# Performance work log

Measured on AMD Instinct MI355X. Metric: run time of the kernel, lower is better.

## Reference

```python
import jax, jax.numpy as jnp
import numpy as np

N_HEADS = 8
TANH_CLIPPING = 10.0
TEMP = 1.0


def setup_inputs() -> dict:
    key = jax.random.key(0)
    ks = jax.random.split(key, 8)
    B, N, D, CTX = 256, 1000, 128, 130
    embeddings = jax.random.normal(ks[0], (B, N, D), dtype=jnp.float32)
    step_context = jax.random.normal(ks[1], (B, 1, CTX), dtype=jnp.float32)
    mask = jax.random.randint(ks[2], (B, 1, N), 0, 2).astype(bool)
    # ensure at least one feasible node per row (node 0 always feasible)
    mask = mask.at[:, :, 0].set(False)
    W_node = jax.random.normal(ks[3], (D, 3 * D), dtype=jnp.float32) * (1.0 / np.sqrt(D))
    W_fixed = jax.random.normal(ks[4], (D, D), dtype=jnp.float32) * (1.0 / np.sqrt(D))
    W_step = jax.random.normal(ks[5], (CTX, D), dtype=jnp.float32) * (1.0 / np.sqrt(CTX))
    W_out = jax.random.normal(ks[6], (D, D), dtype=jnp.float32) * (1.0 / np.sqrt(D))
    return {"embeddings": embeddings, "step_context": step_context, "mask": mask,
            "W_node": W_node, "W_fixed": W_fixed, "W_step": W_step, "W_out": W_out}


def reference(embeddings, step_context, mask, W_node, W_fixed, W_step, W_out):
    # embeddings: [B, N, D], step_context: [B, 1, D+2], mask: [B, 1, N] (True = infeasible)
    B, N, D = embeddings.shape
    H = N_HEADS
    hd = D // H
    # _precompute: fixed context from graph mean, and K/V/logit_key from node embeddings
    graph_embed = embeddings.mean(axis=1)                       # [B, D]
    fixed_context = graph_embed @ W_fixed                       # [B, D]
    kvl = embeddings @ W_node                                   # [B, N, 3D]
    glimpse_k, glimpse_v, logit_k = jnp.split(kvl, 3, axis=-1)  # each [B, N, D]
    # query = fixed context + projected step context             [B, 1, D]
    query = fixed_context[:, None, :] + step_context @ W_step
    # multi-head glimpse attention (q_len = 1)
    q = query.reshape(B, 1, H, hd).transpose(0, 2, 1, 3)        # [B, H, 1, hd]
    K = glimpse_k.reshape(B, N, H, hd).transpose(0, 2, 1, 3)    # [B, H, N, hd]
    V = glimpse_v.reshape(B, N, H, hd).transpose(0, 2, 1, 3)    # [B, H, N, hd]
    compat = jnp.einsum('bhqd,bhnd->bhqn', q, K) / jnp.sqrt(jnp.float32(hd))
    # mask_inner
    compat = jnp.where(mask[:, None, :, :], -jnp.inf, compat)
    attn = jax.nn.softmax(compat, axis=-1)                      # [B, H, 1, N]
    heads = jnp.einsum('bhqn,bhnd->bhqd', attn, V)              # [B, H, 1, hd]
    glimpse = heads.transpose(0, 2, 1, 3).reshape(B, 1, D) @ W_out  # [B, 1, D]
    # single-head logits against logit_key, tanh-clipped
    logits = jnp.einsum('bqd,bnd->bqn', glimpse, logit_k) / jnp.sqrt(jnp.float32(D))
    logits = jnp.tanh(logits) * TANH_CLIPPING
    # mask_logits
    logits = jnp.where(mask, -jnp.inf, logits)
    log_p = jax.nn.log_softmax(logits / TEMP, axis=-1)          # [B, 1, N]
    return log_p
```

## Files before the change

kernel.cpp:

```cpp
#include <hip/hip_runtime.h>
#include <math.h>

#define NN   1000
#define DD   128
#define CTXN 130
#define NEG_BIG (-1.0e30f)

__device__ __forceinline__ float fast_tanh(float a) {
    a = fminf(fmaxf(a, -20.f), 20.f);
    const float ex = __expf(-2.0f * a);
    return (1.0f - ex) / (1.0f + ex);
}


__global__ __launch_bounds__(1024, 4)
void k1_fused(const float* __restrict__ emb, const float* __restrict__ stepc,
              const void* __restrict__ maskp,
              const float* __restrict__ Wn, const float* __restrict__ Wf,
              const float* __restrict__ Ws,
              float* __restrict__ qpt, int* __restrict__ idxv, int* __restrict__ cntv) {
    const int b = blockIdx.x, t = threadIdx.x;
    const int w = t >> 6, lane = t & 63;
    const float* eb = emb + (size_t)b * (NN * DD);
    __shared__ __align__(16) float S[4096];
    __shared__ float s_mean[128], s_q[128];
    __shared__ int s_misint;
    __shared__ unsigned long long s_bal[16];
    __shared__ int s_woff[16];
    if (t == 0) {
        const unsigned char* mb8 = (const unsigned char*)maskp;
        int any = 0;
        for (int k = 0; k < 64; ++k) any |= mb8[4 * k + 1];
        s_misint = (any == 0) ? 1 : 0;
    }
    {
        const int c4 = t & 31, g = t >> 5;
        float4 a = make_float4(0.f, 0.f, 0.f, 0.f);
        for (int r = g; r < NN; r += 32) {
            const float4 v = *(const float4*)(eb + (size_t)r * DD + c4 * 4);
            a.x += v.x; a.y += v.y; a.z += v.z; a.w += v.w;
        }
        ((float4*)S)[g * 32 + c4] = a;
    }
    __syncthreads();
    if (t < 128) {
        float v = 0.f;
        #pragma unroll
        for (int g = 0; g < 32; ++g) v += S[g * 128 + t];
        s_mean[t] = v * (1.0f / (float)NN);
    }
    __syncthreads();
    {
        const int d = t & 127, p = t >> 7;
        float a = 0.f;
        for (int i = 16 * p; i < 16 * p + 16; ++i)
            a = fmaf(s_mean[i], Wf[i * DD + d], a);
        const float* scb = stepc + (size_t)b * CTXN;
        const int c0 = 16 * p, c1 = (p == 7) ? CTXN : 16 * p + 16;
        for (int c = c0; c < c1; ++c)
            a = fmaf(scb[c], Ws[c * DD + d], a);
        S[p * 128 + d] = a;
    }
    __syncthreads();
    if (t < 128) {
        float v = 0.f;
        #pragma unroll
        for (int p = 0; p < 8; ++p) v += S[p * 128 + t];
        s_q[t] = v;
    }
    __syncthreads();
    {
        const int i = t & 127, h = t >> 7;
        float a = 0.f;
        #pragma unroll
        for (int j = 0; j < 16; ++j)
            a = fmaf(Wn[i * 384 + h * 16 + j], s_q[h * 16 + j], a);
        qpt[(size_t)b * 1024 + h * 128 + i] = a * 0.25f;
    }
    {
        const unsigned char* mk8 = (const unsigned char*)maskp + (size_t)b * NN;
        const int* mk32 = (const int*)maskp + (size_t)b * NN;
        int um = 0;
        if (t < NN) um = s_misint ? (mk32[t] == 0) : (mk8[t] == 0);
        const unsigned long long bal = __ballot(um);
        if (lane == 0) s_bal[w] = bal;
        __syncthreads();
        if (t == 0) {
            int o = 0;
            #pragma unroll
            for (int w2 = 0; w2 < 16; ++w2) {
                s_woff[w2] = o;
                o += (int)__popcll(s_bal[w2]);
            }
            cntv[b] = o;
        }
        __syncthreads();
        if (um) {
            const int pos = s_woff[w] +
                (int)__popcll(bal & ((lane == 0) ? 0ULL : (~0ULL >> (64 - lane))));
            idxv[(size_t)b * 1024 + pos] = t;
        }
    }
}

__global__ __launch_bounds__(512, 4)
void kB_stream(const float* __restrict__ emb, const float* __restrict__ qpt,
               const float* __restrict__ Wn,
               const int* __restrict__ idxv, const int* __restrict__ cntv,
               float* __restrict__ headsp, float* __restrict__ stats) {
    const int b = blockIdx.x >> 3, s = blockIdx.x & 7;
    const int t = threadIdx.x, w = t >> 6, lane = t & 63;
    const int rg = lane >> 4, cl = lane & 15;
    const int cnt = cntv[b];
    const int lo = (s * cnt) >> 3;
    const int hi = ((s + 1) * cnt) >> 3;
    const int nrows = hi - lo;
    const float* eb = emb + (size_t)b * (NN * DD);
    __shared__ __align__(16) float s_qpT[1024];
    __shared__ __align__(16) float s_part[8 * 8 * 132];
    __shared__ float s_sumw[64];
    __shared__ int s_idx[128];
    for (int i = t; i < 1024; i += 512) s_qpT[i] = qpt[(size_t)b * 1024 + i];
    if (t < 128) s_idx[t] = (t < nrows) ? idxv[(size_t)b * 1024 + lo + t] : 0;
    __syncthreads();
    const int h0 = 2 * rg, h1 = 2 * rg + 1;
    const float4 qa0 = *(const float4*)&s_qpT[h0 * 128 + cl * 8];
    const float4 qa1 = *(const float4*)&s_qpT[h0 * 128 + cl * 8 + 4];
    const float4 qb0 = *(const float4*)&s_qpT[h1 * 128 + cl * 8];
    const float4 qb1 = *(const float4*)&s_qpT[h1 * 128 + cl * 8 + 4];
    float4 a0A = make_float4(0.f,0.f,0.f,0.f), a0B = a0A;
    float4 a1A = a0A, a1B = a0A;
    float ps0 = 0.f, ps1 = 0.f;
    const int mainIt = nrows >> 3;
    for (int it = 0; it < mainIt; ++it) {
        const int rp = it * 8 + w;
        const int n = s_idx[rp];
        const float4 e0 = *(const float4*)(eb + (size_t)n * DD + cl * 8);
        const float4 e1 = *(const float4*)(eb + (size_t)n * DD + cl * 8 + 4);
        float c0 = e0.x * qa0.x;
        c0 = fmaf(e0.y, qa0.y, c0); c0 = fmaf(e0.z, qa0.z, c0); c0 = fmaf(e0.w, qa0.w, c0);
        c0 = fmaf(e1.x, qa1.x, c0); c0 = fmaf(e1.y, qa1.y, c0);
        c0 = fmaf(e1.z, qa1.z, c0); c0 = fmaf(e1.w, qa1.w, c0);
        float c1 = e0.x * qb0.x;
        c1 = fmaf(e0.y, qb0.y, c1); c1 = fmaf(e0.z, qb0.z, c1); c1 = fmaf(e0.w, qb0.w, c1);
        c1 = fmaf(e1.x, qb1.x, c1); c1 = fmaf(e1.y, qb1.y, c1);
        c1 = fmaf(e1.z, qb1.z, c1); c1 = fmaf(e1.w, qb1.w, c1);
        c0 += __shfl_xor(c0, 1, 16); c1 += __shfl_xor(c1, 1, 16);
        c0 += __shfl_xor(c0, 2, 16); c1 += __shfl_xor(c1, 2, 16);
        c0 += __shfl_xor(c0, 4, 16); c1 += __shfl_xor(c1, 4, 16);
        c0 += __shfl_xor(c0, 8, 16); c1 += __shfl_xor(c1, 8, 16);
        const float p0 = __expf(fminf(c0, 80.f));
        const float p1 = __expf(fminf(c1, 80.f));
        ps0 += p0; ps1 += p1;
        a0A.x = fmaf(p0, e0.x, a0A.x); a0A.y = fmaf(p0, e0.y, a0A.y);
        a0A.z = fmaf(p0, e0.z, a0A.z); a0A.w = fmaf(p0, e0.w, a0A.w);
        a0B.x = fmaf(p0, e1.x, a0B.x); a0B.y = fmaf(p0, e1.y, a0B.y);
        a0B.z = fmaf(p0, e1.z, a0B.z); a0B.w = fmaf(p0, e1.w, a0B.w);
        a1A.x = fmaf(p1, e0.x, a1A.x); a1A.y = fmaf(p1, e0.y, a1A.y);
        a1A.z = fmaf(p1, e0.z, a1A.z); a1A.w = fmaf(p1, e0.w, a1A.w);
        a1B.x = fmaf(p1, e1.x, a1B.x); a1B.y = fmaf(p1, e1.y, a1B.y);
        a1B.z = fmaf(p1, e1.z, a1B.z); a1B.w = fmaf(p1, e1.w, a1B.w);
    }
    if (mainIt * 8 < nrows) {
        const int rp = mainIt * 8 + w;
        const bool valid = (rp < nrows);
        const int n = s_idx[rp & 127];
        float4 e0 = make_float4(0.f,0.f,0.f,0.f), e1 = e0;
        if (valid) {
            e0 = *(const float4*)(eb + (size_t)n * DD + cl * 8);
            e1 = *(const float4*)(eb + (size_t)n * DD + cl * 8 + 4);
        }
        float c0 = e0.x * qa0.x;
        c0 = fmaf(e0.y, qa0.y, c0); c0 = fmaf(e0.z, qa0.z, c0); c0 = fmaf(e0.w, qa0.w, c0);
        c0 = fmaf(e1.x, qa1.x, c0); c0 = fmaf(e1.y, qa1.y, c0);
        c0 = fmaf(e1.z, qa1.z, c0); c0 = fmaf(e1.w, qa1.w, c0);
        float c1 = e0.x * qb0.x;
        c1 = fmaf(e0.y, qb0.y, c1); c1 = fmaf(e0.z, qb0.z, c1); c1 = fmaf(e0.w, qb0.w, c1);
        c1 = fmaf(e1.x, qb1.x, c1); c1 = fmaf(e1.y, qb1.y, c1);
        c1 = fmaf(e1.z, qb1.z, c1); c1 = fmaf(e1.w, qb1.w, c1);
        c0 += __shfl_xor(c0, 1, 16); c1 += __shfl_xor(c1, 1, 16);
        c0 += __shfl_xor(c0, 2, 16); c1 += __shfl_xor(c1, 2, 16);
        c0 += __shfl_xor(c0, 4, 16); c1 += __shfl_xor(c1, 4, 16);
        c0 += __shfl_xor(c0, 8, 16); c1 += __shfl_xor(c1, 8, 16);
        const float p0 = valid ? __expf(fminf(c0, 80.f)) : 0.f;
        const float p1 = valid ? __expf(fminf(c1, 80.f)) : 0.f;
        ps0 += p0; ps1 += p1;
        a0A.x = fmaf(p0, e0.x, a0A.x); a0A.y = fmaf(p0, e0.y, a0A.y);
        a0A.z = fmaf(p0, e0.z, a0A.z); a0A.w = fmaf(p0, e0.w, a0A.w);
        a0B.x = fmaf(p0, e1.x, a0B.x); a0B.y = fmaf(p0, e1.y, a0B.y);
        a0B.z = fmaf(p0, e1.z, a0B.z); a0B.w = fmaf(p0, e1.w, a0B.w);
        a1A.x = fmaf(p1, e0.x, a1A.x); a1A.y = fmaf(p1, e0.y, a1A.y);
        a1A.z = fmaf(p1, e0.z, a1A.z); a1A.w = fmaf(p1, e0.w, a1A.w);
        a1B.x = fmaf(p1, e1.x, a1B.x); a1B.y = fmaf(p1, e1.y, a1B.y);
        a1B.z = fmaf(p1, e1.z, a1B.z); a1B.w = fmaf(p1, e1.w, a1B.w);
    }
    *(float4*)&s_part[(w * 8 + h0) * 132 + cl * 8]     = a0A;
    *(float4*)&s_part[(w * 8 + h0) * 132 + cl * 8 + 4] = a0B;
    *(float4*)&s_part[(w * 8 + h1) * 132 + cl * 8]     = a1A;
    *(float4*)&s_part[(w * 8 + h1) * 132 + cl * 8 + 4] = a1B;
    if (cl == 0) { s_sumw[w * 8 + h0] = ps0; s_sumw[w * 8 + h1] = ps1; }
    __syncthreads();
    float vres0, vres1;
    {
        const int i0 = t, i1 = t + 512;
        const int hA = i0 >> 7, cA = i0 & 127;
        const int hB = i1 >> 7, cB = i1 & 127;
        float v0 = 0.f, v1 = 0.f;
        #pragma unroll
        for (int w2 = 0; w2 < 8; ++w2) {
            v0 += s_part[(w2 * 8 + hA) * 132 + cA];
            v1 += s_part[(w2 * 8 + hB) * 132 + cB];
        }
        vres0 = v0; vres1 = v1;
    }
    __syncthreads();
    s_part[t]       = vres0;
    s_part[t + 512] = vres1;
    __syncthreads();
    {
        const int j = t & 127, p = t >> 7;
        const int h = j >> 4;
        float a = 0.f;
        for (int i = 32 * p; i < 32 * p + 32; ++i)
            a = fmaf(Wn[i * 384 + 128 + j], s_part[h * 128 + i], a);
        s_part[1024 + p * 128 + j] = a;
    }
    __syncthreads();
    if (t < 128)
        headsp[(size_t)b * 1024 + s * 128 + t] =
            s_part[1024 + t] + s_part[1024 + 128 + t] +
            s_part[1024 + 256 + t] + s_part[1024 + 384 + t];
    if (t < 8) {
        float v = 0.f;
        #pragma unroll
        for (int w2 = 0; w2 < 8; ++w2) v += s_sumw[w2 * 8 + t];
        stats[(size_t)b * 64 + s * 8 + t] = v;
    }
}

__global__ __launch_bounds__(1024, 4)
void k4_fused(const float* __restrict__ emb, const float* __restrict__ headsp,
              const float* __restrict__ stats,
              const float* __restrict__ Wn, const float* __restrict__ Wo,
              const int* __restrict__ idxv, const int* __restrict__ cntv,
              float* __restrict__ out) {
    const int b = blockIdx.x, t = threadIdx.x;
    const int w = t >> 6, lane = t & 63;
    const int rg = lane >> 4, cl = lane & 15;
    const float* eb = emb + (size_t)b * (NN * DD);
    __shared__ float s_dinv[8];
    __shared__ __align__(16) float s_red[1024];
    __shared__ float s_h[128], s_gl[128], s_g2[128];
    __shared__ float s_logits[1000];
    __shared__ int s_idxf[1024];
    __shared__ float s_r2[32];
    __shared__ float s_lse;
    const int cnt = cntv[b];
    if (t < NN) s_logits[t] = NEG_BIG;
    s_idxf[t] = (t < cnt) ? idxv[(size_t)b * 1024 + t] : 0;
    if (t < 8) {
        float den = 0.f;
        #pragma unroll
        for (int ss = 0; ss < 8; ++ss) den += stats[(size_t)b * 64 + ss * 8 + t];
        s_dinv[t] = 1.0f / den;
    }
    __syncthreads();
    if (t < 128) {
        float v = 0.f;
        #pragma unroll
        for (int ss = 0; ss < 8; ++ss) v += headsp[(size_t)b * 1024 + ss * 128 + t];
        s_h[t] = v * s_dinv[t >> 4];
    }
    __syncthreads();
    {
        const int d = t & 127, p = t >> 7;
        float a = 0.f;
        for (int j = 16 * p; j < 16 * p + 16; ++j)
            a = fmaf(s_h[j], Wo[j * DD + d], a);
        s_red[p * 128 + d] = a;
    }
    __syncthreads();
    if (t < 128) {
        float v = 0.f;
        #pragma unroll
        for (int p = 0; p < 8; ++p) v += s_red[p * 128 + t];
        s_gl[t] = v;
    }
    __syncthreads();
    {
        const int i = t & 127, p = t >> 7;
        float a = 0.f;
        for (int d = 16 * p; d < 16 * p + 16; ++d)
            a = fmaf(Wn[i * 384 + 256 + d], s_gl[d], a);
        s_red[p * 128 + i] = a;
    }
    __syncthreads();
    if (t < 128) {
        float v = 0.f;
        #pragma unroll
        for (int p = 0; p < 8; ++p) v += s_red[p * 128 + t];
        s_g2[t] = v * 0.08838834764831845f;
    }
    __syncthreads();
    {
        const float4 ga = *(const float4*)&s_g2[cl * 8];
        const float4 gb = *(const float4*)&s_g2[cl * 8 + 4];
        const int mainL = cnt >> 6;
        for (int it = 0; it < mainL; ++it) {
            const int pos = it * 64 + w * 4 + rg;
            const int n = s_idxf[pos];
            const float4 e0 = *(const float4*)(eb + (size_t)n * DD + cl * 8);
            const float4 e1 = *(const float4*)(eb + (size_t)n * DD + cl * 8 + 4);
            float a = e0.x * ga.x;
            a = fmaf(e0.y, ga.y, a);
            a = fmaf(e0.z, ga.z, a);
            a = fmaf(e0.w, ga.w, a);
            a = fmaf(e1.x, gb.x, a);
            a = fmaf(e1.y, gb.y, a);
            a = fmaf(e1.z, gb.z, a);
            a = fmaf(e1.w, gb.w, a);
            a += __shfl_xor(a, 1, 16);
            a += __shfl_xor(a, 2, 16);
            a += __shfl_xor(a, 4, 16);
            a += __shfl_xor(a, 8, 16);
            if (cl == 0)
                s_logits[n] = 10.0f * fast_tanh(a);
        }
        if (mainL * 64 < cnt) {
            const int pos = mainL * 64 + w * 4 + rg;
            const bool valid = (pos < cnt);
            const int n = s_idxf[pos & 1023];
            float a = 0.f;
            if (valid) {
                const float4 e0 = *(const float4*)(eb + (size_t)n * DD + cl * 8);
                const float4 e1 = *(const float4*)(eb + (size_t)n * DD + cl * 8 + 4);
                a = e0.x * ga.x;
                a = fmaf(e0.y, ga.y, a);
                a = fmaf(e0.z, ga.z, a);
                a = fmaf(e0.w, ga.w, a);
                a = fmaf(e1.x, gb.x, a);
                a = fmaf(e1.y, gb.y, a);
                a = fmaf(e1.z, gb.z, a);
                a = fmaf(e1.w, gb.w, a);
            }
            a += __shfl_xor(a, 1, 16);
            a += __shfl_xor(a, 2, 16);
            a += __shfl_xor(a, 4, 16);
            a += __shfl_xor(a, 8, 16);
            if (cl == 0 && valid)
                s_logits[n] = 10.0f * fast_tanh(a);
        }
    }
    __syncthreads();
    {
        float sum = (t < NN) ? __expf(s_logits[t]) : 0.f;
        #pragma unroll
        for (int o = 32; o; o >>= 1) sum += __shfl_xor(sum, o, 64);
        if (lane == 0) s_r2[w] = sum;
        __syncthreads();
        if (t == 0) {
            float ss = 0.f;
            #pragma unroll
            for (int i = 0; i < 16; ++i) ss += s_r2[i];
            s_lse = logf(ss);
        }
        __syncthreads();
        if (t < NN) out[(size_t)b * NN + t] = s_logits[t] - s_lse;
    }
}

extern "C" void kernel_launch(void* const* d_in, const int* in_sizes, int n_in,
                              void* d_out, int out_size, void* d_ws, size_t ws_size,
                              hipStream_t stream) {
    const float* emb   = (const float*)d_in[0];
    const float* stepc = (const float*)d_in[1];
    const void*  mask  = (const void*)d_in[2];
    const float* Wn = (const float*)d_in[3];
    const float* Wf = (const float*)d_in[4];
    const float* Ws = (const float*)d_in[5];
    const float* Wo = (const float*)d_in[6];
    float* out = (float*)d_out;
    const int B = in_sizes[0] / (NN * DD);

    float* wsf = (float*)d_ws;
    const size_t n_qpt   = (size_t)B * 1024;
    const size_t n_hp    = (size_t)B * 1024;
    const size_t n_stats = (size_t)B * 64;
    const size_t n_idx   = (size_t)B * 1024;

    float* qpt    = wsf;
    float* headsp = qpt + n_qpt;
    float* stats  = headsp + n_hp;
    int*   idxv   = (int*)(stats + n_stats);
    int*   cntv   = idxv + n_idx;

    k1_fused <<<B,     1024, 0, stream>>>(emb, stepc, mask, Wn, Wf, Ws, qpt, idxv, cntv);
    kB_stream<<<B * 8, 512,  0, stream>>>(emb, qpt, Wn, idxv, cntv, headsp, stats);
    k4_fused <<<B,     1024, 0, stream>>>(emb, headsp, stats, Wn, Wo, idxv, cntv, out);
}
```

Before: 78.31 us.

## Split graph-mean pass across 8 blocks per batch and recompute query/index lists per block

The first kernel, which ran one 1024-thread block per batch row to read all embeddings for the mean, becomes a lightweight partial-sum kernel launched with 8 blocks per batch row. This raises parallelism for the full-embedding read. The query projection and the compaction of feasible node indices move into the streaming kernel, and each of its 8 blocks per batch row recomputes them redundantly. The final kernel rebuilds the index list from the mask itself. The qpt/idxv/cnt global round trips go away in exchange for redundant per-block matrix-vector work and mask scans.

```diff
diff --git a/kernel.cpp b/kernel.cpp
--- a/kernel.cpp
+++ b/kernel.cpp
@@ -13,116 +13,124 @@
 }
 
 
-__global__ __launch_bounds__(1024, 4)
-void k1_fused(const float* __restrict__ emb, const float* __restrict__ stepc,
-              const void* __restrict__ maskp,
-              const float* __restrict__ Wn, const float* __restrict__ Wf,
-              const float* __restrict__ Ws,
-              float* __restrict__ qpt, int* __restrict__ idxv, int* __restrict__ cntv) {
-    const int b = blockIdx.x, t = threadIdx.x;
-    const int w = t >> 6, lane = t & 63;
+__global__ __launch_bounds__(256, 8)
+void k1p_meanpart(const float* __restrict__ emb, float* __restrict__ meanp) {
+    const int b = blockIdx.x >> 3, s = blockIdx.x & 7;
+    const int t = threadIdx.x;
     const float* eb = emb + (size_t)b * (NN * DD);
-    __shared__ __align__(16) float S[4096];
-    __shared__ float s_mean[128], s_q[128];
-    __shared__ int s_misint;
+    __shared__ __align__(16) float s_red[8 * 128];
+    const int c4 = t & 31, rg = t >> 5;
+    float4 a = make_float4(0.f, 0.f, 0.f, 0.f);
+    for (int nl = rg; nl < 125; nl += 8) {
+        const float4 v = *(const float4*)(eb + (size_t)(s * 125 + nl) * DD + c4 * 4);
+        a.x += v.x; a.y += v.y; a.z += v.z; a.w += v.w;
+    }
+    ((float4*)s_red)[rg * 32 + c4] = a;
+    __syncthreads();
+    if (t < 128) {
+        float v = 0.f;
+        #pragma unroll
+        for (int g = 0; g < 8; ++g) v += s_red[g * 128 + t];
+        meanp[(size_t)b * 1024 + s * 128 + t] = v;
+    }
+}
+
+__global__ __launch_bounds__(512, 4)
+void kB_stream(const float* __restrict__ emb, const float* __restrict__ meanp,
+               const float* __restrict__ stepc, const void* __restrict__ maskp,
+               const float* __restrict__ Wn, const float* __restrict__ Wf,
+               const float* __restrict__ Ws,
+               float* __restrict__ headsp, float* __restrict__ stats) {
+    const int b = blockIdx.x >> 3, s = blockIdx.x & 7;
+    const int t = threadIdx.x, w = t >> 6, lane = t & 63;
+    const int rg = lane >> 4, cl = lane & 15;
+    const float* eb = emb + (size_t)b * (NN * DD);
+    __shared__ __align__(16) float s_qpT[1024];
+    __shared__ __align__(16) float s_part[8 * 8 * 132];
+    __shared__ float s_sumw[64];
+    __shared__ int s_idx[128];
     __shared__ unsigned long long s_bal[16];
     __shared__ int s_woff[16];
+    __shared__ int s_cnt, s_misint;
+    float* s_mean = s_part;
+    float* s_q    = s_part + 128;
+    float* s_scr  = s_part + 256;
     if (t == 0) {
         const unsigned char* mb8 = (const unsigned char*)maskp;
         int any = 0;
         for (int k = 0; k < 64; ++k) any |= mb8[4 * k + 1];
         s_misint = (any == 0) ? 1 : 0;
     }
-    {
-        const int c4 = t & 31, g = t >> 5;
-        float4 a = make_float4(0.f, 0.f, 0.f, 0.f);
-        for (int r = g; r < NN; r += 32) {
-            const float4 v = *(const float4*)(eb + (size_t)r * DD + c4 * 4);
-            a.x += v.x; a.y += v.y; a.z += v.z; a.w += v.w;
-        }
-        ((float4*)S)[g * 32 + c4] = a;
-    }
-    __syncthreads();
     if (t < 128) {
         float v = 0.f;
         #pragma unroll
-        for (int g = 0; g < 32; ++g) v += S[g * 128 + t];
+        for (int g = 0; g < 8; ++g) v += meanp[(size_t)b * 1024 + g * 128 + t];
         s_mean[t] = v * (1.0f / (float)NN);
     }
     __syncthreads();
     {
         const int d = t & 127, p = t >> 7;
         float a = 0.f;
-        for (int i = 16 * p; i < 16 * p + 16; ++i)
+        for (int i = 32 * p; i < 32 * p + 32; ++i)
             a = fmaf(s_mean[i], Wf[i * DD + d], a);
         const float* scb = stepc + (size_t)b * CTXN;
-        const int c0 = 16 * p, c1 = (p == 7) ? CTXN : 16 * p + 16;
+        const int c0 = 32 * p, c1 = (p == 3) ? CTXN : 32 * p + 32;
         for (int c = c0; c < c1; ++c)
             a = fmaf(scb[c], Ws[c * DD + d], a);
-        S[p * 128 + d] = a;
-    }
-    __syncthreads();
-    if (t < 128) {
-        float v = 0.f;
-        #pragma unroll
-        for (int p = 0; p < 8; ++p) v += S[p * 128 + t];
-        s_q[t] = v;
-    }
-    __syncthreads();
-    {
-        const int i = t & 127, h = t >> 7;
-        float a = 0.f;
-        #pragma unroll
-        for (int j = 0; j < 16; ++j)
-            a = fmaf(Wn[i * 384 + h * 16 + j], s_q[h * 16 + j], a);
-        qpt[(size_t)b * 1024 + h * 128 + i] = a * 0.25f;
+        s_scr[p * 128 + d] = a;
+    }
+    __syncthreads();
+    if (t < 128) s_q[t] = s_scr[t] + s_scr[128 + t] + s_scr[256 + t] + s_scr[384 + t];
+    __syncthreads();
+    {
+        const int i = t & 127, p = t >> 7;
+        #pragma unroll
+        for (int u = 0; u < 2; ++u) {
+            const int h = p + 4 * u;
+            float a = 0.f;
+            #pragma unroll
+            for (int j = 0; j < 16; ++j)
+                a = fmaf(Wn[i * 384 + h * 16 + j], s_q[h * 16 + j], a);
+            s_qpT[h * 128 + i] = a * 0.25f;
+        }
     }
     {
         const unsigned char* mk8 = (const unsigned char*)maskp + (size_t)b * NN;
         const int* mk32 = (const int*)maskp + (size_t)b * NN;
-        int um = 0;
-        if (t < NN) um = s_misint ? (mk32[t] == 0) : (mk8[t] == 0);
-        const unsigned long long bal = __ballot(um);
-        if (lane == 0) s_bal[w] = bal;
+        const int misint = s_misint;
+        #pragma unroll
+        for (int r = 0; r < 2; ++r) {
+            const int gi = r * 512 + t;
+            int um = 0;
+            if (gi < NN) um = misint ? (mk32[gi] == 0) : (mk8[gi] == 0);
+            const unsigned long long bal = __ballot(um);
+            if (lane == 0) s_bal[r * 8 + w] = bal;
+        }
         __syncthreads();
         if (t == 0) {
             int o = 0;
             #pragma unroll
-            for (int w2 = 0; w2 < 16; ++w2) {
-                s_woff[w2] = o;
-                o += (int)__popcll(s_bal[w2]);
+            for (int k = 0; k < 16; ++k) { s_woff[k] = o; o += (int)__popcll(s_bal[k]); }
+            s_cnt = o;
+        }
+        __syncthreads();
+        const int cnt = s_cnt;
+        const int lo = (s * cnt) >> 3, hi = ((s + 1) * cnt) >> 3;
+        #pragma unroll
+        for (int r = 0; r < 2; ++r) {
+            const int gi = r * 512 + t;
+            const unsigned long long bal = s_bal[r * 8 + w];
+            if ((bal >> lane) & 1ULL) {
+                const int pos = s_woff[r * 8 + w] +
+                    (int)__popcll(bal & ((lane == 0) ? 0ULL : (~0ULL >> (64 - lane))));
+                if (pos >= lo && pos < hi) s_idx[pos - lo] = gi;
             }
-            cntv[b] = o;
-        }
-        __syncthreads();
-        if (um) {
-            const int pos = s_woff[w] +
-                (int)__popcll(bal & ((lane == 0) ? 0ULL : (~0ULL >> (64 - lane))));
-            idxv[(size_t)b * 1024 + pos] = t;
-        }
-    }
-}
-
-__global__ __launch_bounds__(512, 4)
-void kB_stream(const float* __restrict__ emb, const float* __restrict__ qpt,
-               const float* __restrict__ Wn,
-               const int* __restrict__ idxv, const int* __restrict__ cntv,
-               float* __restrict__ headsp, float* __restrict__ stats) {
-    const int b = blockIdx.x >> 3, s = blockIdx.x & 7;
-    const int t = threadIdx.x, w = t >> 6, lane = t & 63;
-    const int rg = lane >> 4, cl = lane & 15;
-    const int cnt = cntv[b];
-    const int lo = (s * cnt) >> 3;
-    const int hi = ((s + 1) * cnt) >> 3;
+        }
+    }
+    __syncthreads();
+    const int cnt = s_cnt;
+    const int lo = (s * cnt) >> 3, hi = ((s + 1) * cnt) >> 3;
     const int nrows = hi - lo;
-    const float* eb = emb + (size_t)b * (NN * DD);
-    __shared__ __align__(16) float s_qpT[1024];
-    __shared__ __align__(16) float s_part[8 * 8 * 132];
-    __shared__ float s_sumw[64];
-    __shared__ int s_idx[128];
-    for (int i = t; i < 1024; i += 512) s_qpT[i] = qpt[(size_t)b * 1024 + i];
-    if (t < 128) s_idx[t] = (t < nrows) ? idxv[(size_t)b * 1024 + lo + t] : 0;
-    __syncthreads();
     const int h0 = 2 * rg, h1 = 2 * rg + 1;
     const float4 qa0 = *(const float4*)&s_qpT[h0 * 128 + cl * 8];
     const float4 qa1 = *(const float4*)&s_qpT[h0 * 128 + cl * 8 + 4];
@@ -194,6 +202,7 @@
         a1B.x = fmaf(p1, e1.x, a1B.x); a1B.y = fmaf(p1, e1.y, a1B.y);
         a1B.z = fmaf(p1, e1.z, a1B.z); a1B.w = fmaf(p1, e1.w, a1B.w);
     }
+    __syncthreads();
     *(float4*)&s_part[(w * 8 + h0) * 132 + cl * 8]     = a0A;
     *(float4*)&s_part[(w * 8 + h0) * 132 + cl * 8 + 4] = a0B;
     *(float4*)&s_part[(w * 8 + h1) * 132 + cl * 8]     = a1A;
@@ -240,9 +249,8 @@
 
 __global__ __launch_bounds__(1024, 4)
 void k4_fused(const float* __restrict__ emb, const float* __restrict__ headsp,
-              const float* __restrict__ stats,
+              const float* __restrict__ stats, const void* __restrict__ maskp,
               const float* __restrict__ Wn, const float* __restrict__ Wo,
-              const int* __restrict__ idxv, const int* __restrict__ cntv,
               float* __restrict__ out) {
     const int b = blockIdx.x, t = threadIdx.x;
     const int w = t >> 6, lane = t & 63;
@@ -255,9 +263,16 @@
     __shared__ int s_idxf[1024];
     __shared__ float s_r2[32];
     __shared__ float s_lse;
-    const int cnt = cntv[b];
+    __shared__ unsigned long long s_bal[16];
+    __shared__ int s_woff[16];
+    __shared__ int s_cnt, s_misint;
     if (t < NN) s_logits[t] = NEG_BIG;
-    s_idxf[t] = (t < cnt) ? idxv[(size_t)b * 1024 + t] : 0;
+    if (t == 0) {
+        const unsigned char* mb8 = (const unsigned char*)maskp;
+        int any = 0;
+        for (int k = 0; k < 64; ++k) any |= mb8[4 * k + 1];
+        s_misint = (any == 0) ? 1 : 0;
+    }
     if (t < 8) {
         float den = 0.f;
         #pragma unroll
@@ -265,6 +280,27 @@
         s_dinv[t] = 1.0f / den;
     }
     __syncthreads();
+    {
+        const unsigned char* mk8 = (const unsigned char*)maskp + (size_t)b * NN;
+        const int* mk32 = (const int*)maskp + (size_t)b * NN;
+        int um = 0;
+        if (t < NN) um = s_misint ? (mk32[t] == 0) : (mk8[t] == 0);
+        const unsigned long long bal = __ballot(um);
+        if (lane == 0) s_bal[w] = bal;
+        __syncthreads();
+        if (t == 0) {
+            int o = 0;
+            #pragma unroll
+            for (int k = 0; k < 16; ++k) { s_woff[k] = o; o += (int)__popcll(s_bal[k]); }
+            s_cnt = o;
+        }
+        __syncthreads();
+        if (um) {
+            const int pos = s_woff[w] +
+                (int)__popcll(bal & ((lane == 0) ? 0ULL : (~0ULL >> (64 - lane))));
+            s_idxf[pos] = t;
+        }
+    }
     if (t < 128) {
         float v = 0.f;
         #pragma unroll
@@ -303,6 +339,7 @@
     }
     __syncthreads();
     {
+        const int cnt = s_cnt;
         const float4 ga = *(const float4*)&s_g2[cl * 8];
         const float4 gb = *(const float4*)&s_g2[cl * 8 + 4];
         const int mainL = cnt >> 6;
@@ -383,18 +420,15 @@
     const int B = in_sizes[0] / (NN * DD);
 
     float* wsf = (float*)d_ws;
-    const size_t n_qpt   = (size_t)B * 1024;
+    const size_t n_meanp = (size_t)B * 1024;
     const size_t n_hp    = (size_t)B * 1024;
-    const size_t n_stats = (size_t)B * 64;
-    const size_t n_idx   = (size_t)B * 1024;
-
-    float* qpt    = wsf;
-    float* headsp = qpt + n_qpt;
+
+    float* meanp  = wsf;
+    float* headsp = meanp + n_meanp;
     float* stats  = headsp + n_hp;
-    int*   idxv   = (int*)(stats + n_stats);
-    int*   cntv   = idxv + n_idx;
-
-    k1_fused <<<B,     1024, 0, stream>>>(emb, stepc, mask, Wn, Wf, Ws, qpt, idxv, cntv);
-    kB_stream<<<B * 8, 512,  0, stream>>>(emb, qpt, Wn, idxv, cntv, headsp, stats);
-    k4_fused <<<B,     1024, 0, stream>>>(emb, headsp, stats, Wn, Wo, idxv, cntv, out);
+
+    k1p_meanpart<<<B * 8, 256, 0, stream>>>(emb, meanp);
+    kB_stream   <<<B * 8, 512, 0, stream>>>(emb, meanp, stepc, mask, Wn, Wf, Ws,
+                                            headsp, stats);
+    k4_fused    <<<B,     1024, 0, stream>>>(emb, headsp, stats, mask, Wn, Wo, out);
 }
```

Result: slower. 115.6 us (+47.6%).
